# Kernel optimization log

Measured on AMD Instinct MI355X. Metric: run time of the kernel, lower is better.

The kernel has to match this reference:

```python
import jax, jax.numpy as jnp
import numpy as np

B, T, HID, DIM, K, NQ = 8, 4096, 512, 256, 1024, 8
COMMIT_W = 1.0  # cfg commitment_weight


def setup_inputs() -> dict:
    key = jax.random.key(0)
    ks = jax.random.split(key, 4)
    rn = lambda k, shape, scale: jax.random.normal(k, shape, dtype=jnp.float32) * scale
    return {
        "x": rn(ks[0], (B, T, HID), 1.0),
        "W_in": rn(ks[1], (DIM, HID), HID ** -0.5),
        "b_in": jnp.zeros((DIM,), jnp.float32),
        "W_out": rn(ks[2], (HID, DIM), DIM ** -0.5),
        "b_out": jnp.zeros((HID,), jnp.float32),
        "codebooks": rn(ks[3], (NQ, K, DIM), 1.0),
    }


def _rvq(h, codebooks):
    """Residual VQ over NQ quantizers. h: [B,T,D]; codebooks: [NQ,K,D]."""
    def step(residual, cb):
        # squared-euclidean distance to each code: [B,T,K]
        d = (jnp.sum(residual * residual, axis=-1, keepdims=True)
             - 2.0 * jnp.einsum("btd,kd->btk", residual, cb)
             + jnp.sum(cb * cb, axis=-1))
        idx = jnp.argmin(d, axis=-1)                 # [B,T] nearest code
        q = cb[idx]                                   # [B,T,D] gather
        commit = COMMIT_W * jnp.mean((jax.lax.stop_gradient(q) - residual) ** 2)
        q_st = residual + jax.lax.stop_gradient(q - residual)  # straight-through
        return residual - q_st, (q_st, commit)

    _, (q_all, losses) = jax.lax.scan(step, h, codebooks)
    return q_all, losses  # [NQ,B,T,D], [NQ]


def reference(x, W_in, b_in, W_out, b_out, codebooks):
    h = x @ W_in.T + b_in                            # proj_in: [B,T,DIM]
    # torch code transposes to [B,D,T] for rvq and back; pure layout, math identical in [B,T,D]
    q_all, losses = _rvq(h, codebooks)
    quantized_out = q_all.sum(axis=0)                # sum of per-layer quantized
    out = quantized_out @ W_out.T + b_out            # proj_out: [B,T,HID]
    q1 = q_all[0]
    q2 = q_all[1]
    com = losses.mean()
    return out, q1, q2, com
```

## Files before the change

### kernel.cpp

```cpp
#include <hip/hip_runtime.h>

#define BT     32768
#define HIDDEN 512
#define DDIM   256
#define KCODE  1024
#define NQUANT 8

typedef _Float16 f16;
typedef _Float16 f16x8 __attribute__((ext_vector_type(8)));
typedef float f32x4 __attribute__((ext_vector_type(4)));
typedef float f32x8 __attribute__((ext_vector_type(8)));

#define LO_SCALE 64.0f
#define LO_INV   0.015625f

__global__ __launch_bounds__(256) void cnorm_kernel(const float* __restrict__ cb,
                                                    float* __restrict__ cnorm) {
  __shared__ float red[256];
  const int code = blockIdx.x;
  const float v = cb[(size_t)code * DDIM + threadIdx.x];
  red[threadIdx.x] = v * v;
  __syncthreads();
  for (int s = 128; s > 0; s >>= 1) {
    if (threadIdx.x < s) red[threadIdx.x] += red[threadIdx.x + s];
    __syncthreads();
  }
  if (threadIdx.x == 0) cnorm[code] = red[0];
}

__global__ __launch_bounds__(256) void cbext_conv(const float* __restrict__ cb,
                                                  f16* __restrict__ cbext) {
  const size_t idx = (size_t)blockIdx.x * 256 + threadIdx.x;
  const size_t c = idx >> 8;
  const int d = (int)(idx & 255);
  const float v = cb[idx];
  const f16 hi = (f16)v;
  cbext[c * 512 + d] = hi;
  cbext[c * 512 + 256 + d] = (f16)((v - (float)hi) * LO_SCALE);
}

__global__ __launch_bounds__(256) void bext_conv(const float* __restrict__ W,
                                                 f16* __restrict__ Wext,
                                                 int N, int K) {
  const int idx = blockIdx.x * 256 + threadIdx.x;
  if (idx >= N * K) return;
  const int n = idx / K, k = idx - n * K;
  const float v = W[idx];
  const f16 hi = (f16)v;
  Wext[(size_t)n * 2 * K + k] = hi;
  Wext[(size_t)n * 2 * K + K + k] = (f16)((v - (float)hi) * LO_SCALE);
}

__global__ void zero2(float* commitAcc, unsigned* bar) {
  commitAcc[0] = 0.f;
  bar[0] = 0u;
}

__global__ void finalize_com(const float* __restrict__ a, float* __restrict__ o) {
  o[0] = a[0] * (1.0f / (float)((size_t)NQUANT * BT * DDIM));
}

__device__ __forceinline__ void phase_barrier(unsigned* bar, unsigned gen,
                                              unsigned nblk) {
  __syncthreads();
  if (threadIdx.x == 0) {
    __threadfence();
    atomicAdd(bar, 1u);
    const unsigned target = gen * nblk;
    int spins = 0;
    while (__hip_atomic_load(bar, __ATOMIC_RELAXED, __HIP_MEMORY_SCOPE_AGENT) < target &&
           spins < 16384) {
      ++spins;
      __builtin_amdgcn_s_sleep(4);
    }
  }
  __syncthreads();
}

__global__ __launch_bounds__(512) void rvq_fused6(
    const f16* __restrict__ rext, const f16* __restrict__ cbext,
    const float* __restrict__ cbf32, const float* __restrict__ cnorm,
    float* __restrict__ qsum, float* __restrict__ q1, float* __restrict__ q2,
    float* __restrict__ commitAcc, unsigned* __restrict__ bar) {
  __shared__ __align__(16) f16 Bs[2][64][512];
  __shared__ float redc[512];
  const int tid = threadIdx.x;
  const int w = tid >> 6, l = tid & 63;
  const int lj = l & 15, li = l >> 4;
  const int m0 = blockIdx.x * 128;
  const int row = m0 + w * 16 + lj;
  const int key = (lj & 7) << 4;

  f16x8 af[16];
#pragma unroll
  for (int s = 0; s < 16; ++s)
    af[s] = *(const f16x8*)&rext[(size_t)row * 512 + s * 32 + li * 8];

  float csum = 0.f;

#pragma unroll 1
  for (int nq = 0; nq < NQUANT; ++nq) {
    if (nq > 0) phase_barrier(bar, (unsigned)nq, gridDim.x);
    const f16* cbq = cbext + (size_t)nq * KCODE * 512;
    const float* cnq = cnorm + nq * KCODE;

    auto STAGE = [&](int chunk, int buf) {
#pragma unroll
      for (int q = 0; q < 8; ++q) {
        const int r = w * 8 + q;
        const int code = chunk * 64 + r;
        const char* src = (const char*)(cbq + ((size_t)code << 9)) +
                          ((l * 16) ^ ((r & 7) << 4));
        __builtin_amdgcn_global_load_lds(
            (const __attribute__((address_space(1))) void*)src,
            (__attribute__((address_space(3))) void*)&Bs[buf][r][0], 16, 0, 0);
      }
    };

    float bval[4]; int bidxr[4];
#pragma unroll
    for (int j = 0; j < 4; ++j) { bval[j] = 3.0e38f; bidxr[j] = 0; }

    STAGE(0, 0);
    __syncthreads();
    int buf = 0;

#pragma unroll 1
    for (int c = 0; c < 16; ++c) {
      if (c < 15) STAGE(c + 1, buf ^ 1);
      f32x4 acc[4];
#pragma unroll
      for (int n = 0; n < 4; ++n) acc[n] = (f32x4){0.f, 0.f, 0.f, 0.f};

#pragma unroll
      for (int t = 0; t < 12; ++t) {
        const int tl = (t < 4) ? t : (t < 8 ? t - 4 : t - 8);
        const int roff = (t < 4) ? 512 : 0;
        const int abase = (t >= 4 && t < 8) ? (8 + 2 * tl) : (2 * tl);
        f16x8 bf[4][2];
#pragma unroll
        for (int n = 0; n < 4; ++n) {
          const int rr = n * 16 + lj;
#pragma unroll
          for (int kk = 0; kk < 2; ++kk) {
            const int boff = roff + tl * 128 + kk * 64 + li * 16;
            bf[n][kk] = *(const f16x8*)((const char*)&Bs[buf][rr][0] + (boff ^ key));
          }
        }
#pragma unroll
        for (int n = 0; n < 4; ++n)
#pragma unroll
          for (int kk = 0; kk < 2; ++kk)
            acc[n] = __builtin_amdgcn_mfma_f32_16x16x32_f16(
                af[abase + kk], bf[n][kk], acc[n], 0, 0, 0);
        if (t == 7) {
#pragma unroll
          for (int n = 0; n < 4; ++n)
#pragma unroll
            for (int j = 0; j < 4; ++j) acc[n][j] *= LO_INV;
        }
      }
#pragma unroll
      for (int n = 0; n < 4; ++n) {
        const int cl = c * 64 + n * 16 + lj;
        const float cn = cnq[cl];
#pragma unroll
        for (int j = 0; j < 4; ++j) {
          const float d = cn - 2.0f * acc[n][j];
          if (d < bval[j]) { bval[j] = d; bidxr[j] = cl; }
        }
      }
      __syncthreads();
      buf ^= 1;
    }

#pragma unroll
    for (int off = 1; off < 16; off <<= 1) {
#pragma unroll
      for (int j = 0; j < 4; ++j) {
        const float ov = __shfl_xor(bval[j], off);
        const int oi = __shfl_xor(bidxr[j], off);
        if (ov < bval[j] || (ov == bval[j] && oi < bidxr[j])) {
          bval[j] = ov; bidxr[j] = oi;
        }
      }
    }
    const int src = (lj >> 2) * 16;
    const int c0 = __shfl(bidxr[0], src);
    const int c1 = __shfl(bidxr[1], src);
    const int c2 = __shfl(bidxr[2], src);
    const int c3 = __shfl(bidxr[3], src);
    const int sel = lj & 3;
    const int myCode = (sel == 0) ? c0 : (sel == 1) ? c1 : (sel == 2) ? c2 : c3;

    const float* qrow = cbf32 + ((size_t)nq * KCODE + myCode) * DDIM;
#pragma unroll
    for (int s = 0; s < 8; ++s) {
      const f32x8 qv = *(const f32x8*)&qrow[s * 32 + li * 8];
      f16x8 h = af[s], lo = af[8 + s];
#pragma unroll
      for (int i = 0; i < 8; ++i) {
        const float rold = (float)h[i] + (float)lo[i] * LO_INV;
        const float diff = qv[i] - rold;
        csum += diff * diff;
        const float rnew = rold - qv[i];
        const f16 nh = (f16)rnew;
        h[i] = nh;
        lo[i] = (f16)((rnew - (float)nh) * LO_SCALE);
      }
      af[s] = h; af[8 + s] = lo;
      if (nq == 0)
        *(f32x8*)&q1[(size_t)row * DDIM + s * 32 + li * 8] = qv;
      if (nq == 1)
        *(f32x8*)&q2[(size_t)row * DDIM + s * 32 + li * 8] = qv;
    }
  }

#pragma unroll
  for (int s = 0; s < 8; ++s) {
    const f16x8 hh = *(const f16x8*)&rext[(size_t)row * 512 + s * 32 + li * 8];
    const f16x8 hl = *(const f16x8*)&rext[(size_t)row * 512 + 256 + s * 32 + li * 8];
    f32x8 o;
#pragma unroll
    for (int i = 0; i < 8; ++i)
      o[i] = ((float)hh[i] + (float)hl[i] * LO_INV) -
             ((float)af[s][i] + (float)af[8 + s][i] * LO_INV);
    *(f32x8*)&qsum[(size_t)row * DDIM + s * 32 + li * 8] = o;
  }

  redc[tid] = csum;
  __syncthreads();
  for (int s = 256; s > 0; s >>= 1) {
    if (tid < s) redc[tid] += redc[tid + s];
    __syncthreads();
  }
  if (tid == 0) atomicAdd(commitAcc, redc[0]);
}

template <int K, bool WEXT>
__global__ __launch_bounds__(512) void proj3(
    const float* __restrict__ A, const f16* __restrict__ Bext,
    const float* __restrict__ bias, float* __restrict__ Cout,
    f16* __restrict__ CextOut, int Ntot) {
  __shared__ __align__(16) f16 Bs[128][512];
  const int tid = threadIdx.x;
  const int w = tid >> 6, l = tid & 63;
  const int lj = l & 15, li = l >> 4;
  const int m0 = blockIdx.x * 128;
  const int n0 = blockIdx.y * 128;
  const int row_t = m0 + w * 16 + lj;
  const int key = (lj & 7) << 4;

  f32x4 acc[8], acc2[8];
#pragma unroll
  for (int n = 0; n < 8; ++n) {
    acc[n] = (f32x4){0.f, 0.f, 0.f, 0.f};
    acc2[n] = (f32x4){0.f, 0.f, 0.f, 0.f};
  }

#pragma unroll 1
  for (int p = 0; p < K / 256; ++p) {
    __syncthreads();
#pragma unroll
    for (int q = 0; q < 16; ++q) {
      const int r = w * 16 + q;
      const int nrow = n0 + r;
      const int byteoff = (l * 16) ^ ((r & 7) << 4);
      const char* hi_base =
          (const char*)Bext + ((size_t)nrow * 2 * K + p * 256) * 2;
      const char* lo_base =
          (const char*)Bext + ((size_t)nrow * 2 * K + K + p * 256) * 2;
      const char* src = (byteoff < 512) ? hi_base + byteoff
                                        : lo_base + (byteoff - 512);
      __builtin_amdgcn_global_load_lds(
          (const __attribute__((address_space(1))) void*)src,
          (__attribute__((address_space(3))) void*)&Bs[r][0], 16, 0, 0);
    }
    f16x8 ahi[8], alo[8];
#pragma unroll
    for (int s = 0; s < 8; ++s) {
      const f32x8 v = *(const f32x8*)&A[(size_t)row_t * K + p * 256 + s * 32 + li * 8];
      f16x8 h, lo;
#pragma unroll
      for (int i = 0; i < 8; ++i) {
        const f16 hh = (f16)v[i];
        h[i] = hh;
        lo[i] = (f16)((v[i] - (float)hh) * LO_SCALE);
      }
      ahi[s] = h; alo[s] = lo;
    }
    __syncthreads();

#pragma unroll
    for (int t = 0; t < 12; ++t) {
      const int tl = (t < 4) ? t : (t < 8 ? t - 4 : t - 8);
      const int roff = (t < 4) ? 512 : 0;
#pragma unroll
      for (int n = 0; n < 8; ++n) {
        const int rr = n * 16 + lj;
#pragma unroll
        for (int kk = 0; kk < 2; ++kk) {
          const int boff = roff + tl * 128 + kk * 64 + li * 16;
          const f16x8 bf = *(const f16x8*)((const char*)&Bs[rr][0] + (boff ^ key));
          if (t < 4)
            acc2[n] = __builtin_amdgcn_mfma_f32_16x16x32_f16(ahi[2 * tl + kk], bf, acc2[n], 0, 0, 0);
          else if (t < 8)
            acc2[n] = __builtin_amdgcn_mfma_f32_16x16x32_f16(alo[2 * tl + kk], bf, acc2[n], 0, 0, 0);
          else
            acc[n] = __builtin_amdgcn_mfma_f32_16x16x32_f16(ahi[2 * tl + kk], bf, acc[n], 0, 0, 0);
        }
      }
    }
  }

#pragma unroll
  for (int n = 0; n < 8; ++n) {
    const int ncol = n0 + n * 16 + lj;
    const float bb = bias[ncol];
#pragma unroll
    for (int j = 0; j < 4; ++j) {
      const int tok = m0 + w * 16 + li * 4 + j;
      const float vv = acc[n][j] + acc2[n][j] * LO_INV + bb;
      if (WEXT) {
        const f16 hh = (f16)vv;
        CextOut[(size_t)tok * 512 + ncol] = hh;
        CextOut[(size_t)tok * 512 + 256 + ncol] = (f16)((vv - (float)hh) * LO_SCALE);
      } else {
        Cout[(size_t)tok * Ntot + ncol] = vv;
      }
    }
  }
}

extern "C" void kernel_launch(void* const* d_in, const int* in_sizes, int n_in,
                              void* d_out, int out_size, void* d_ws, size_t ws_size,
                              hipStream_t stream) {
  (void)in_sizes; (void)n_in; (void)out_size; (void)ws_size;
  const float* x     = (const float*)d_in[0];
  const float* W_in  = (const float*)d_in[1];
  const float* b_in  = (const float*)d_in[2];
  const float* W_out = (const float*)d_in[3];
  const float* b_out = (const float*)d_in[4];
  const float* cbs   = (const float*)d_in[5];

  float* out = (float*)d_out;
  float* q1  = out + (size_t)BT * HIDDEN;
  float* q2  = q1 + (size_t)BT * DDIM;
  float* com = q2 + (size_t)BT * DDIM;

  f16*   rext      = (f16*)d_ws;
  float* qsum      = (float*)(rext + (size_t)BT * 512);
  f16*   cbext     = (f16*)(qsum + (size_t)BT * DDIM);
  f16*   W_inext   = cbext + (size_t)NQUANT * KCODE * 512;
  f16*   W_outext  = W_inext + (size_t)DDIM * 1024;
  float* cnorm     = (float*)(W_outext + (size_t)HIDDEN * 512);
  float* commitAcc = cnorm + NQUANT * KCODE;
  unsigned* bar    = (unsigned*)(commitAcc + 1);

  cnorm_kernel<<<NQUANT * KCODE, 256, 0, stream>>>(cbs, cnorm);
  cbext_conv<<<NQUANT * KCODE, 256, 0, stream>>>(cbs, cbext);
  bext_conv<<<(DDIM * HIDDEN + 255) / 256, 256, 0, stream>>>(W_in, W_inext, DDIM, HIDDEN);
  bext_conv<<<(HIDDEN * DDIM + 255) / 256, 256, 0, stream>>>(W_out, W_outext, HIDDEN, DDIM);
  proj3<HIDDEN, true><<<dim3(BT / 128, DDIM / 128), 512, 0, stream>>>(
      x, W_inext, b_in, nullptr, rext, DDIM);
  zero2<<<1, 1, 0, stream>>>(commitAcc, bar);
  rvq_fused6<<<BT / 128, 512, 0, stream>>>(rext, cbext, cbs, cnorm,
                                           qsum, q1, q2, commitAcc, bar);
  proj3<DDIM, false><<<dim3(BT / 128, HIDDEN / 128), 512, 0, stream>>>(
      qsum, W_outext, b_out, out, nullptr, HIDDEN);
  finalize_com<<<1, 1, 0, stream>>>(commitAcc, com);
}
```

Measured before the change: 775.5 us.

## Shrink RVQ blocks to 64 rows and split main/correction accumulators

The fused RVQ kernel now uses 256-thread blocks covering 64 rows, with 32-code chunks, halving the LDS tile so more blocks fit per CU and the grid doubles to 512 blocks. The three-pass split-fp16 MFMA sequence is replaced by separate main and correction accumulators, which removes the mid-loop rescale and interleaves two independent MFMA chains. The cost is twice as many blocks hitting the grid-wide spin barrier and each codebook chunk being staged by more blocks, which raises L2 traffic.

```diff
diff --git a/kernel.cpp b/kernel.cpp
--- a/kernel.cpp
+++ b/kernel.cpp
@@ -77,17 +77,17 @@
   __syncthreads();
 }
 
-__global__ __launch_bounds__(512) void rvq_fused6(
+__global__ __launch_bounds__(256) void rvq_fused10(
     const f16* __restrict__ rext, const f16* __restrict__ cbext,
     const float* __restrict__ cbf32, const float* __restrict__ cnorm,
     float* __restrict__ qsum, float* __restrict__ q1, float* __restrict__ q2,
     float* __restrict__ commitAcc, unsigned* __restrict__ bar) {
-  __shared__ __align__(16) f16 Bs[2][64][512];
-  __shared__ float redc[512];
+  __shared__ __align__(16) f16 Bs[2][32][512];
+  __shared__ float redc[256];
   const int tid = threadIdx.x;
   const int w = tid >> 6, l = tid & 63;
   const int lj = l & 15, li = l >> 4;
-  const int m0 = blockIdx.x * 128;
+  const int m0 = blockIdx.x * 64;
   const int row = m0 + w * 16 + lj;
   const int key = (lj & 7) << 4;
 
@@ -108,7 +108,7 @@
 #pragma unroll
       for (int q = 0; q < 8; ++q) {
         const int r = w * 8 + q;
-        const int code = chunk * 64 + r;
+        const int code = chunk * 32 + r;
         const char* src = (const char*)(cbq + ((size_t)code << 9)) +
                           ((l * 16) ^ ((r & 7) << 4));
         __builtin_amdgcn_global_load_lds(
@@ -126,47 +126,59 @@
     int buf = 0;
 
 #pragma unroll 1
-    for (int c = 0; c < 16; ++c) {
-      if (c < 15) STAGE(c + 1, buf ^ 1);
-      f32x4 acc[4];
-#pragma unroll
-      for (int n = 0; n < 4; ++n) acc[n] = (f32x4){0.f, 0.f, 0.f, 0.f};
-
-#pragma unroll
-      for (int t = 0; t < 12; ++t) {
-        const int tl = (t < 4) ? t : (t < 8 ? t - 4 : t - 8);
-        const int roff = (t < 4) ? 512 : 0;
-        const int abase = (t >= 4 && t < 8) ? (8 + 2 * tl) : (2 * tl);
-        f16x8 bf[4][2];
-#pragma unroll
-        for (int n = 0; n < 4; ++n) {
+    for (int c = 0; c < 32; ++c) {
+      if (c < 31) STAGE(c + 1, buf ^ 1);
+      f32x4 accM[2], accC[2];
+#pragma unroll
+      for (int n = 0; n < 2; ++n) {
+        accM[n] = (f32x4){0.f, 0.f, 0.f, 0.f};
+        accC[n] = (f32x4){0.f, 0.f, 0.f, 0.f};
+      }
+
+#pragma unroll
+      for (int tl = 0; tl < 4; ++tl) {
+#pragma unroll
+        for (int n = 0; n < 2; ++n) {
           const int rr = n * 16 + lj;
+          f16x8 bf[2];
 #pragma unroll
           for (int kk = 0; kk < 2; ++kk) {
-            const int boff = roff + tl * 128 + kk * 64 + li * 16;
-            bf[n][kk] = *(const f16x8*)((const char*)&Bs[buf][rr][0] + (boff ^ key));
+            const int boff = 512 + tl * 128 + kk * 64 + li * 16;
+            bf[kk] = *(const f16x8*)((const char*)&Bs[buf][rr][0] + (boff ^ key));
           }
-        }
-#pragma unroll
-        for (int n = 0; n < 4; ++n)
 #pragma unroll
           for (int kk = 0; kk < 2; ++kk)
-            acc[n] = __builtin_amdgcn_mfma_f32_16x16x32_f16(
-                af[abase + kk], bf[n][kk], acc[n], 0, 0, 0);
-        if (t == 7) {
-#pragma unroll
-          for (int n = 0; n < 4; ++n)
-#pragma unroll
-            for (int j = 0; j < 4; ++j) acc[n][j] *= LO_INV;
-        }
-      }
-#pragma unroll
-      for (int n = 0; n < 4; ++n) {
-        const int cl = c * 64 + n * 16 + lj;
+            accC[n] = __builtin_amdgcn_mfma_f32_16x16x32_f16(
+                af[2 * tl + kk], bf[kk], accC[n], 0, 0, 0);
+        }
+      }
+#pragma unroll
+      for (int tl = 0; tl < 4; ++tl) {
+#pragma unroll
+        for (int n = 0; n < 2; ++n) {
+          const int rr = n * 16 + lj;
+          f16x8 bf[2];
+#pragma unroll
+          for (int kk = 0; kk < 2; ++kk) {
+            const int boff = tl * 128 + kk * 64 + li * 16;
+            bf[kk] = *(const f16x8*)((const char*)&Bs[buf][rr][0] + (boff ^ key));
+          }
+#pragma unroll
+          for (int kk = 0; kk < 2; ++kk) {
+            accC[n] = __builtin_amdgcn_mfma_f32_16x16x32_f16(
+                af[8 + 2 * tl + kk], bf[kk], accC[n], 0, 0, 0);
+            accM[n] = __builtin_amdgcn_mfma_f32_16x16x32_f16(
+                af[2 * tl + kk], bf[kk], accM[n], 0, 0, 0);
+          }
+        }
+      }
+#pragma unroll
+      for (int n = 0; n < 2; ++n) {
+        const int cl = c * 32 + n * 16 + lj;
         const float cn = cnq[cl];
 #pragma unroll
         for (int j = 0; j < 4; ++j) {
-          const float d = cn - 2.0f * acc[n][j];
+          const float d = cn - 2.0f * (accM[n][j] + accC[n][j] * LO_INV);
           if (d < bval[j]) { bval[j] = d; bidxr[j] = cl; }
         }
       }
@@ -230,7 +242,7 @@
 
   redc[tid] = csum;
   __syncthreads();
-  for (int s = 256; s > 0; s >>= 1) {
+  for (int s = 128; s > 0; s >>= 1) {
     if (tid < s) redc[tid] += redc[tid + s];
     __syncthreads();
   }
@@ -364,7 +376,7 @@
   proj3<HIDDEN, true><<<dim3(BT / 128, DDIM / 128), 512, 0, stream>>>(
       x, W_inext, b_in, nullptr, rext, DDIM);
   zero2<<<1, 1, 0, stream>>>(commitAcc, bar);
-  rvq_fused6<<<BT / 128, 512, 0, stream>>>(rext, cbext, cbs, cnorm,
+  rvq_fused10<<<BT / 64, 256, 0, stream>>>(rext, cbext, cbs, cnorm,
                                            qsum, q1, q2, commitAcc, bar);
   proj3<DDIM, false><<<dim3(BT / 128, HIDDEN / 128), 512, 0, stream>>>(
       qsum, W_outext, b_out, out, nullptr, HIDDEN);
```

Measured after the change: 909.3 us. 17.3% more time.
